# Kernel tuning notes

Measured on AMD Instinct MI355X. Metric: run time of the kernel, lower is better.

The kernel has to match this reference:

```python
import jax, jax.numpy as jnp
import numpy as np

NUM_NODES = 100000
D = 256            # node_hidden_dim
H = 256            # edge_hidden_dim
P = 524288         # num_pairs


def setup_inputs() -> dict:
    key = jax.random.key(0)
    k1, k2, k3, k4, k5, k6 = jax.random.split(key, 6)
    h_nodes = jax.random.normal(k1, (NUM_NODES, D), dtype=jnp.float32)
    dst = jax.random.randint(k2, (P,), 0, NUM_NODES, dtype=jnp.int64)
    src = jax.random.randint(k3, (P,), 0, NUM_NODES, dtype=jnp.int64)
    # Bias-free MLP weights, stored as [in, out] so forward is x @ W
    s1 = 1.0 / np.sqrt(2 * D)
    s2 = 1.0 / np.sqrt(H)
    W1 = jax.random.uniform(k4, (2 * D, H), jnp.float32, -s1, s1)
    W2 = jax.random.uniform(k5, (H, H), jnp.float32, -s2, s2)
    W3 = jax.random.uniform(k6, (H, 2), jnp.float32, -s2, s2)
    return {"h_nodes": h_nodes, "dst": dst, "src": src, "W1": W1, "W2": W2, "W3": W3}


def reference(h_nodes, dst, src, W1, W2, W3):
    # gather src/dst embeddings and concat -> [P, 2D]
    h_pair = jnp.concatenate([h_nodes[dst], h_nodes[src]], axis=-1)
    x = jax.nn.relu(h_pair @ W1)   # [P, H]
    x = jax.nn.relu(x @ W2)        # [P, H]
    return x @ W3                  # [P, 2] edge logits
```

## Files before the change

kernel.cpp:

```cpp
#include <hip/hip_runtime.h>
#include <stdint.h>

typedef __attribute__((ext_vector_type(8))) short short8;
typedef __attribute__((ext_vector_type(4))) float floatx4;

__device__ __forceinline__ unsigned short f2bf(float x) {
  unsigned int u = __float_as_uint(x);
  u += 0x7fffu + ((u >> 16) & 1u);
  return (unsigned short)(u >> 16);
}
__device__ __forceinline__ float bf2f(unsigned short b) {
  return __uint_as_float(((unsigned int)b) << 16);
}

__global__ void hcvt_kernel(const float* __restrict__ h,
                            unsigned short* __restrict__ o, int total8) {
  int u = blockIdx.x * 256 + threadIdx.x;
  if (u >= total8) return;
  const float4* h4 = (const float4*)h;
  float4 v0 = h4[u * 2], v1 = h4[u * 2 + 1];
  short8 s;
  s[0] = (short)f2bf(v0.x); s[1] = (short)f2bf(v0.y);
  s[2] = (short)f2bf(v0.z); s[3] = (short)f2bf(v0.w);
  s[4] = (short)f2bf(v1.x); s[5] = (short)f2bf(v1.y);
  s[6] = (short)f2bf(v1.z); s[7] = (short)f2bf(v1.w);
  ((short8*)o)[u] = s;
}

__global__ void wfrag_kernel(const float* __restrict__ W,
                             unsigned short* __restrict__ out, int total) {
  int u = blockIdx.x * 256 + threadIdx.x;
  if (u >= total) return;
  int j   = u & 7;
  int kq  = (u >> 3) & 3;
  int n   = (u >> 5) & 255;
  int k32 = u >> 13;
  int k   = k32 * 32 + kq * 8 + j;
  out[u] = f2bf(W[k * 256 + n]);
}

__global__ __launch_bounds__(256, 2)
void edge_mlp2(const unsigned short* __restrict__ hbf,
               const int* __restrict__ dst,
               const int* __restrict__ src,
               const unsigned short* __restrict__ W1F,
               const unsigned short* __restrict__ W2F,
               const float* __restrict__ W3,
               float* __restrict__ out) {
  __shared__ unsigned short A[64 * 512];
  __shared__ float w3s[512];
  __shared__ int ioff[128];
  unsigned short* X = A;

  const int t = threadIdx.x, lane = t & 63, w = t >> 6;
  const int lq = lane >> 4, lm = lane & 15;
  const int m0 = blockIdx.x * 64;

  if (t < 64)       ioff[t] = dst[m0 + t];
  else if (t < 128) ioff[t] = src[m0 + t - 64];
  w3s[t] = W3[t];
  w3s[t + 256] = W3[t + 256];
  __syncthreads();

  {
    const int c = lane, half = (c >= 32) ? 64 : 0, cc = c & 31;
    short8 g[16];
#pragma unroll
    for (int it = 0; it < 16; ++it) {
      int node = ioff[half + it * 4 + w];
      g[it] = ((const short8*)hbf)[node * 32 + cc];
    }
#pragma unroll
    for (int it = 0; it < 16; ++it) {
      int r = it * 4 + w;
      *(short8*)&A[r * 512 + ((c ^ (r & 7)) << 3)] = g[it];
    }
  }

  floatx4 acc[4][4];
#pragma unroll
  for (int i = 0; i < 4; ++i)
#pragma unroll
    for (int j = 0; j < 4; ++j) acc[i][j] = (floatx4)(0.0f);
  __syncthreads();

  const short8* B1 = (const short8*)W1F;
  const short8* B2 = (const short8*)W2F;

  {
    short8 bq[4][4];
#pragma unroll
    for (int s = 0; s < 4; ++s)
#pragma unroll
      for (int jt = 0; jt < 4; ++jt)
        bq[s][jt] = B1[(s * 256 + w * 64 + jt * 16 + lm) * 4 + lq];

#pragma unroll
    for (int s = 0; s < 16; ++s) {
#pragma unroll
      for (int i = 0; i < 4; ++i) {
        int r = i * 16 + lm, cch = s * 4 + lq;
        short8 af = *(const short8*)&A[r * 512 + ((cch ^ (r & 7)) << 3)];
#pragma unroll
        for (int j = 0; j < 4; ++j)
          acc[i][j] = __builtin_amdgcn_mfma_f32_16x16x32_bf16(af, bq[s & 3][j], acc[i][j], 0, 0, 0);
      }
      if (s < 12)
#pragma unroll
        for (int jt = 0; jt < 4; ++jt)
          bq[s & 3][jt] = B1[((s + 4) * 256 + w * 64 + jt * 16 + lm) * 4 + lq];
    }
  }
  __syncthreads();
#pragma unroll
  for (int i = 0; i < 4; ++i) {
    int row0 = i * 16 + lq * 4;
#pragma unroll
    for (int j = 0; j < 4; ++j) {
      int col = w * 64 + j * 16 + lm, c8 = col >> 3, ce = col & 7;
#pragma unroll
      for (int rg = 0; rg < 4; ++rg) {
        int row = row0 + rg;
        float v = acc[i][j][rg];
        v = v > 0.0f ? v : 0.0f;
        X[row * 256 + (((c8 ^ (row & 7)) << 3) | ce)] = f2bf(v);
      }
    }
  }
#pragma unroll
  for (int i = 0; i < 4; ++i)
#pragma unroll
    for (int j = 0; j < 4; ++j) acc[i][j] = (floatx4)(0.0f);
  __syncthreads();

  {
    short8 bq[4][4];
#pragma unroll
    for (int s = 0; s < 4; ++s)
#pragma unroll
      for (int jt = 0; jt < 4; ++jt)
        bq[s][jt] = B2[(s * 256 + w * 64 + jt * 16 + lm) * 4 + lq];

#pragma unroll
    for (int s = 0; s < 8; ++s) {
#pragma unroll
      for (int i = 0; i < 4; ++i) {
        int r = i * 16 + lm, cch = s * 4 + lq;
        short8 af = *(const short8*)&X[r * 256 + ((cch ^ (r & 7)) << 3)];
#pragma unroll
        for (int j = 0; j < 4; ++j)
          acc[i][j] = __builtin_amdgcn_mfma_f32_16x16x32_bf16(af, bq[s & 3][j], acc[i][j], 0, 0, 0);
      }
      if (s < 4)
#pragma unroll
        for (int jt = 0; jt < 4; ++jt)
          bq[s & 3][jt] = B2[((s + 4) * 256 + w * 64 + jt * 16 + lm) * 4 + lq];
    }
  }
  __syncthreads();
#pragma unroll
  for (int i = 0; i < 4; ++i) {
    int row0 = i * 16 + lq * 4;
#pragma unroll
    for (int j = 0; j < 4; ++j) {
      int col = w * 64 + j * 16 + lm, c8 = col >> 3, ce = col & 7;
#pragma unroll
      for (int rg = 0; rg < 4; ++rg) {
        int row = row0 + rg;
        float v = acc[i][j][rg];
        v = v > 0.0f ? v : 0.0f;
        X[row * 256 + (((c8 ^ (row & 7)) << 3) | ce)] = f2bf(v);
      }
    }
  }
  __syncthreads();

  {
    int r = t >> 2, o = (t >> 1) & 1, hh = t & 1;
    float s = 0.0f;
#pragma unroll
    for (int it = 0; it < 16; ++it) {
      int c = hh * 16 + it;
      short8 xv = *(const short8*)&X[r * 256 + ((c ^ (r & 7)) << 3)];
#pragma unroll
      for (int e = 0; e < 8; ++e)
        s += bf2f((unsigned short)xv[e]) * w3s[((c << 3) + e) * 2 + o];
    }
    s += __shfl_xor(s, 1);
    if (hh == 0) out[(m0 + r) * 2 + o] = s;
  }
}

__global__ __launch_bounds__(256, 2)
void edge_mlp_fb(const float* __restrict__ h,
                 const int* __restrict__ dst,
                 const int* __restrict__ src,
                 const unsigned short* __restrict__ W1F,
                 const unsigned short* __restrict__ W2F,
                 const float* __restrict__ W3,
                 float* __restrict__ out) {
  __shared__ unsigned short A[64 * 512];
  __shared__ float w3s[512];
  __shared__ int ioff[128];
  unsigned short* X = A;
  const int t = threadIdx.x, lane = t & 63, w = t >> 6;
  const int lq = lane >> 4, lm = lane & 15;
  const int m0 = blockIdx.x * 64;
  if (t < 64) ioff[t] = dst[m0 + t];
  else if (t < 128) ioff[t] = src[m0 + t - 64];
  w3s[t] = W3[t];
  w3s[t + 256] = W3[t + 256];
  __syncthreads();
  {
    const int c = lane, half = (c >= 32) ? 64 : 0, cc = c & 31;
#pragma unroll
    for (int it = 0; it < 16; ++it) {
      int r = it * 4 + w;
      int node = ioff[half + r];
      const float4* h4 = (const float4*)h;
      float4 v0 = h4[node * 64 + cc * 2], v1 = h4[node * 64 + cc * 2 + 1];
      short8 v;
      v[0] = (short)f2bf(v0.x); v[1] = (short)f2bf(v0.y);
      v[2] = (short)f2bf(v0.z); v[3] = (short)f2bf(v0.w);
      v[4] = (short)f2bf(v1.x); v[5] = (short)f2bf(v1.y);
      v[6] = (short)f2bf(v1.z); v[7] = (short)f2bf(v1.w);
      *(short8*)&A[r * 512 + ((c ^ (r & 7)) << 3)] = v;
    }
  }
  floatx4 acc[4][4];
#pragma unroll
  for (int i = 0; i < 4; ++i)
#pragma unroll
    for (int j = 0; j < 4; ++j) acc[i][j] = (floatx4)(0.0f);
  __syncthreads();
  const short8* B1 = (const short8*)W1F;
  const short8* B2 = (const short8*)W2F;
#pragma unroll
  for (int k32 = 0; k32 < 16; ++k32) {
    short8 b[4], af[4];
#pragma unroll
    for (int jt = 0; jt < 4; ++jt)
      b[jt] = B1[(k32 * 256 + w * 64 + jt * 16 + lm) * 4 + lq];
#pragma unroll
    for (int i = 0; i < 4; ++i) {
      int r = i * 16 + lm, c = k32 * 4 + lq;
      af[i] = *(const short8*)&A[r * 512 + ((c ^ (r & 7)) << 3)];
    }
#pragma unroll
    for (int i = 0; i < 4; ++i)
#pragma unroll
      for (int j = 0; j < 4; ++j)
        acc[i][j] = __builtin_amdgcn_mfma_f32_16x16x32_bf16(af[i], b[j], acc[i][j], 0, 0, 0);
  }
  __syncthreads();
#pragma unroll
  for (int i = 0; i < 4; ++i) {
    int row0 = i * 16 + lq * 4;
#pragma unroll
    for (int j = 0; j < 4; ++j) {
      int col = w * 64 + j * 16 + lm, c8 = col >> 3, ce = col & 7;
#pragma unroll
      for (int rg = 0; rg < 4; ++rg) {
        int row = row0 + rg;
        float v = acc[i][j][rg];
        v = v > 0.0f ? v : 0.0f;
        X[row * 256 + (((c8 ^ (row & 7)) << 3) | ce)] = f2bf(v);
      }
    }
  }
#pragma unroll
  for (int i = 0; i < 4; ++i)
#pragma unroll
    for (int j = 0; j < 4; ++j) acc[i][j] = (floatx4)(0.0f);
  __syncthreads();
#pragma unroll
  for (int k32 = 0; k32 < 8; ++k32) {
    short8 b[4], af[4];
#pragma unroll
    for (int jt = 0; jt < 4; ++jt)
      b[jt] = B2[(k32 * 256 + w * 64 + jt * 16 + lm) * 4 + lq];
#pragma unroll
    for (int i = 0; i < 4; ++i) {
      int r = i * 16 + lm, c = k32 * 4 + lq;
      af[i] = *(const short8*)&X[r * 256 + ((c ^ (r & 7)) << 3)];
    }
#pragma unroll
    for (int i = 0; i < 4; ++i)
#pragma unroll
      for (int j = 0; j < 4; ++j)
        acc[i][j] = __builtin_amdgcn_mfma_f32_16x16x32_bf16(af[i], b[j], acc[i][j], 0, 0, 0);
  }
  __syncthreads();
#pragma unroll
  for (int i = 0; i < 4; ++i) {
    int row0 = i * 16 + lq * 4;
#pragma unroll
    for (int j = 0; j < 4; ++j) {
      int col = w * 64 + j * 16 + lm, c8 = col >> 3, ce = col & 7;
#pragma unroll
      for (int rg = 0; rg < 4; ++rg) {
        int row = row0 + rg;
        float v = acc[i][j][rg];
        v = v > 0.0f ? v : 0.0f;
        X[row * 256 + (((c8 ^ (row & 7)) << 3) | ce)] = f2bf(v);
      }
    }
  }
  __syncthreads();
  {
    int r = t >> 2, o = (t >> 1) & 1, hh = t & 1;
    float s = 0.0f;
#pragma unroll
    for (int it = 0; it < 16; ++it) {
      int c = hh * 16 + it;
      short8 xv = *(const short8*)&X[r * 256 + ((c ^ (r & 7)) << 3)];
#pragma unroll
      for (int e = 0; e < 8; ++e)
        s += bf2f((unsigned short)xv[e]) * w3s[((c << 3) + e) * 2 + o];
    }
    s += __shfl_xor(s, 1);
    if (hh == 0) out[(m0 + r) * 2 + o] = s;
  }
}

extern "C" void kernel_launch(void* const* d_in, const int* in_sizes, int n_in,
                              void* d_out, int out_size, void* d_ws, size_t ws_size,
                              hipStream_t stream) {
  const float* h   = (const float*)d_in[0];
  const int*   dst = (const int*)d_in[1];
  const int*   src = (const int*)d_in[2];
  const float* W1  = (const float*)d_in[3];
  const float* W2  = (const float*)d_in[4];
  const float* W3  = (const float*)d_in[5];
  float* out = (float*)d_out;

  const int h_elems = in_sizes[0];
  const int n_pairs = in_sizes[1];
  const int ntiles  = n_pairs / 64;

  const size_t hbf_elems = (size_t)h_elems;
  const bool use_hbf = ws_size >= (hbf_elems + 131072 + 65536) * sizeof(unsigned short);

  unsigned short* HBF = (unsigned short*)d_ws;
  unsigned short* W1F = use_hbf ? HBF + hbf_elems : (unsigned short*)d_ws;
  unsigned short* W2F = W1F + 131072;

  wfrag_kernel<<<512, 256, 0, stream>>>(W1, W1F, 131072);
  wfrag_kernel<<<256, 256, 0, stream>>>(W2, W2F, 65536);

  if (use_hbf) {
    int total8 = h_elems / 8;
    hcvt_kernel<<<(total8 + 255) / 256, 256, 0, stream>>>(h, HBF, total8);
    edge_mlp2<<<ntiles, 256, 0, stream>>>(HBF, dst, src, W1F, W2F, W3, out);
  } else {
    edge_mlp_fb<<<ntiles, 256, 0, stream>>>(h, dst, src, W1F, W2F, W3, out);
  }
}
```

Baseline: 416.3 us.

## Merge prep kernels, use MFMA for final layer, change LDS swizzle

Combines the W1/W2 fragment conversion and the h-to-bf16 conversion into a single prep launch, and adds a padded bf16 W3 fragment so the final 256x2 projection runs as one MFMA chain per wave instead of a scalar dot product with shared-memory W3. The LDS XOR swizzle is changed to also depend on row bit 3, which aims to reduce bank conflicts. The second-layer output is written to a separate LDS region. Together these aim to cut launch overhead, the scalar tail, and LDS conflicts, at the cost of an extra workspace buffer and a final MFMA that mostly computes zero padding.

```diff
diff --git a/kernel.cpp b/kernel.cpp
--- a/kernel.cpp
+++ b/kernel.cpp
@@ -2,6 +2,7 @@
 #include <stdint.h>
 
 typedef __attribute__((ext_vector_type(8))) short short8;
+typedef __attribute__((ext_vector_type(4))) short short4v;
 typedef __attribute__((ext_vector_type(4))) float floatx4;
 
 __device__ __forceinline__ unsigned short f2bf(float x) {
@@ -12,183 +13,205 @@
 __device__ __forceinline__ float bf2f(unsigned short b) {
   return __uint_as_float(((unsigned int)b) << 16);
 }
-
-__global__ void hcvt_kernel(const float* __restrict__ h,
-                            unsigned short* __restrict__ o, int total8) {
-  int u = blockIdx.x * 256 + threadIdx.x;
-  if (u >= total8) return;
-  const float4* h4 = (const float4*)h;
-  float4 v0 = h4[u * 2], v1 = h4[u * 2 + 1];
-  short8 s;
-  s[0] = (short)f2bf(v0.x); s[1] = (short)f2bf(v0.y);
-  s[2] = (short)f2bf(v0.z); s[3] = (short)f2bf(v0.w);
-  s[4] = (short)f2bf(v1.x); s[5] = (short)f2bf(v1.y);
-  s[6] = (short)f2bf(v1.z); s[7] = (short)f2bf(v1.w);
-  ((short8*)o)[u] = s;
+__device__ __forceinline__ int sw3(int r) { return (r & 7) ^ (((r >> 3) & 1) * 3); }
+
+__global__ void prep_kernel(const float* __restrict__ h, const float* __restrict__ W1,
+                            const float* __restrict__ W2, const float* __restrict__ W3,
+                            unsigned short* __restrict__ HBF, unsigned short* __restrict__ W1F,
+                            unsigned short* __restrict__ W2F, unsigned short* __restrict__ W3F,
+                            int nh4) {
+  const int t = threadIdx.x;
+  int b = blockIdx.x;
+  if (b < 512) {
+    int u = b * 256 + t;
+    int j = u & 7, kq = (u >> 3) & 3, n = (u >> 5) & 255, k32 = u >> 13;
+    W1F[u] = f2bf(W1[(k32 * 32 + kq * 8 + j) * 256 + n]);
+    return;
+  }
+  b -= 512;
+  if (b < 256) {
+    int u = b * 256 + t;
+    int j = u & 7, kq = (u >> 3) & 3, n = (u >> 5) & 255, k32 = u >> 13;
+    W2F[u] = f2bf(W2[(k32 * 32 + kq * 8 + j) * 256 + n]);
+    return;
+  }
+  b -= 256;
+  if (b < 16) {
+    int u = b * 256 + t;
+    int j = u & 7, L = (u >> 3) & 63, k32 = u >> 9;
+    int n = L & 15, kq = L >> 4;
+    W3F[u] = (n < 2) ? f2bf(W3[(k32 * 32 + kq * 8 + j) * 2 + n]) : (unsigned short)0;
+    return;
+  }
+  b -= 16;
+  int u = b * 256 + t;
+  if (u < nh4) {
+    float4 v = ((const float4*)h)[u];
+    short4v s;
+    s[0] = (short)f2bf(v.x); s[1] = (short)f2bf(v.y);
+    s[2] = (short)f2bf(v.z); s[3] = (short)f2bf(v.w);
+    ((short4v*)HBF)[u] = s;
+  }
+}
+
+__global__ __launch_bounds__(256, 2)
+void edge_mlp3(const unsigned short* __restrict__ hbf,
+               const int* __restrict__ dst,
+               const int* __restrict__ src,
+               const unsigned short* __restrict__ W1F,
+               const unsigned short* __restrict__ W2F,
+               const unsigned short* __restrict__ W3F,
+               float* __restrict__ out) {
+  __shared__ unsigned short A[64 * 512];
+  __shared__ int ioff[128];
+  unsigned short* X  = A;
+  unsigned short* X2 = A + 16384;
+
+  const int t = threadIdx.x, lane = t & 63, w = t >> 6;
+  const int lq = lane >> 4, lm = lane & 15;
+  const int m0 = blockIdx.x * 64;
+
+  if (t < 64)       ioff[t] = dst[m0 + t];
+  else if (t < 128) ioff[t] = src[m0 + t - 64];
+  __syncthreads();
+
+  {
+    const int c = lane, half = (c >= 32) ? 64 : 0, cc = c & 31;
+    short8 g[16];
+#pragma unroll
+    for (int it = 0; it < 16; ++it) {
+      int node = ioff[half + it * 4 + w];
+      g[it] = ((const short8*)hbf)[node * 32 + cc];
+    }
+#pragma unroll
+    for (int it = 0; it < 16; ++it) {
+      int r = it * 4 + w;
+      *(short8*)&A[r * 512 + ((c ^ sw3(r)) << 3)] = g[it];
+    }
+  }
+
+  floatx4 acc[4][4];
+#pragma unroll
+  for (int i = 0; i < 4; ++i)
+#pragma unroll
+    for (int j = 0; j < 4; ++j) acc[i][j] = (floatx4)(0.0f);
+  __syncthreads();
+
+  const short8* B1 = (const short8*)W1F;
+  const short8* B2 = (const short8*)W2F;
+
+  {
+    short8 bq[4][4];
+#pragma unroll
+    for (int s = 0; s < 4; ++s)
+#pragma unroll
+      for (int jt = 0; jt < 4; ++jt)
+        bq[s][jt] = B1[(s * 256 + w * 64 + jt * 16 + lm) * 4 + lq];
+
+#pragma unroll
+    for (int s = 0; s < 16; ++s) {
+#pragma unroll
+      for (int i = 0; i < 4; ++i) {
+        int r = i * 16 + lm, cch = s * 4 + lq;
+        short8 af = *(const short8*)&A[r * 512 + ((cch ^ sw3(r)) << 3)];
+#pragma unroll
+        for (int j = 0; j < 4; ++j)
+          acc[i][j] = __builtin_amdgcn_mfma_f32_16x16x32_bf16(af, bq[s & 3][j], acc[i][j], 0, 0, 0);
+      }
+      if (s < 12)
+#pragma unroll
+        for (int jt = 0; jt < 4; ++jt)
+          bq[s & 3][jt] = B1[((s + 4) * 256 + w * 64 + jt * 16 + lm) * 4 + lq];
+    }
+  }
+  __syncthreads();
+#pragma unroll
+  for (int i = 0; i < 4; ++i) {
+    int row0 = i * 16 + lq * 4;
+#pragma unroll
+    for (int j = 0; j < 4; ++j) {
+      int col = w * 64 + j * 16 + lm, c8 = col >> 3, ce = col & 7;
+#pragma unroll
+      for (int rg = 0; rg < 4; ++rg) {
+        int row = row0 + rg;
+        float v = acc[i][j][rg];
+        v = v > 0.0f ? v : 0.0f;
+        X[row * 256 + (((c8 ^ sw3(row)) << 3) | ce)] = f2bf(v);
+      }
+    }
+  }
+#pragma unroll
+  for (int i = 0; i < 4; ++i)
+#pragma unroll
+    for (int j = 0; j < 4; ++j) acc[i][j] = (floatx4)(0.0f);
+  __syncthreads();
+
+  {
+    short8 bq[4][4];
+#pragma unroll
+    for (int s = 0; s < 4; ++s)
+#pragma unroll
+      for (int jt = 0; jt < 4; ++jt)
+        bq[s][jt] = B2[(s * 256 + w * 64 + jt * 16 + lm) * 4 + lq];
+
+#pragma unroll
+    for (int s = 0; s < 8; ++s) {
+#pragma unroll
+      for (int i = 0; i < 4; ++i) {
+        int r = i * 16 + lm, cch = s * 4 + lq;
+        short8 af = *(const short8*)&X[r * 256 + ((cch ^ sw3(r)) << 3)];
+#pragma unroll
+        for (int j = 0; j < 4; ++j)
+          acc[i][j] = __builtin_amdgcn_mfma_f32_16x16x32_bf16(af, bq[s & 3][j], acc[i][j], 0, 0, 0);
+      }
+      if (s < 4)
+#pragma unroll
+        for (int jt = 0; jt < 4; ++jt)
+          bq[s & 3][jt] = B2[((s + 4) * 256 + w * 64 + jt * 16 + lm) * 4 + lq];
+    }
+  }
+  __syncthreads();
+#pragma unroll
+  for (int i = 0; i < 4; ++i) {
+    int row0 = i * 16 + lq * 4;
+#pragma unroll
+    for (int j = 0; j < 4; ++j) {
+      int col = w * 64 + j * 16 + lm, c8 = col >> 3, ce = col & 7;
+#pragma unroll
+      for (int rg = 0; rg < 4; ++rg) {
+        int row = row0 + rg;
+        float v = acc[i][j][rg];
+        v = v > 0.0f ? v : 0.0f;
+        X2[row * 256 + (((c8 ^ sw3(row)) << 3) | ce)] = f2bf(v);
+      }
+    }
+  }
+  __syncthreads();
+
+  {
+    floatx4 a3 = (floatx4)(0.0f);
+    const short8* B3 = (const short8*)W3F;
+#pragma unroll
+    for (int s = 0; s < 8; ++s) {
+      short8 b3 = B3[s * 64 + lane];
+      int r = w * 16 + lm, cch = s * 4 + lq;
+      short8 af = *(const short8*)&X2[r * 256 + ((cch ^ sw3(r)) << 3)];
+      a3 = __builtin_amdgcn_mfma_f32_16x16x32_bf16(af, b3, a3, 0, 0, 0);
+    }
+    if (lm < 2) {
+#pragma unroll
+      for (int rg = 0; rg < 4; ++rg)
+        out[(m0 + w * 16 + lq * 4 + rg) * 2 + lm] = a3[rg];
+    }
+  }
 }
 
 __global__ void wfrag_kernel(const float* __restrict__ W,
                              unsigned short* __restrict__ out, int total) {
   int u = blockIdx.x * 256 + threadIdx.x;
   if (u >= total) return;
-  int j   = u & 7;
-  int kq  = (u >> 3) & 3;
-  int n   = (u >> 5) & 255;
-  int k32 = u >> 13;
-  int k   = k32 * 32 + kq * 8 + j;
-  out[u] = f2bf(W[k * 256 + n]);
-}
-
-__global__ __launch_bounds__(256, 2)
-void edge_mlp2(const unsigned short* __restrict__ hbf,
-               const int* __restrict__ dst,
-               const int* __restrict__ src,
-               const unsigned short* __restrict__ W1F,
-               const unsigned short* __restrict__ W2F,
-               const float* __restrict__ W3,
-               float* __restrict__ out) {
-  __shared__ unsigned short A[64 * 512];
-  __shared__ float w3s[512];
-  __shared__ int ioff[128];
-  unsigned short* X = A;
-
-  const int t = threadIdx.x, lane = t & 63, w = t >> 6;
-  const int lq = lane >> 4, lm = lane & 15;
-  const int m0 = blockIdx.x * 64;
-
-  if (t < 64)       ioff[t] = dst[m0 + t];
-  else if (t < 128) ioff[t] = src[m0 + t - 64];
-  w3s[t] = W3[t];
-  w3s[t + 256] = W3[t + 256];
-  __syncthreads();
-
-  {
-    const int c = lane, half = (c >= 32) ? 64 : 0, cc = c & 31;
-    short8 g[16];
-#pragma unroll
-    for (int it = 0; it < 16; ++it) {
-      int node = ioff[half + it * 4 + w];
-      g[it] = ((const short8*)hbf)[node * 32 + cc];
-    }
-#pragma unroll
-    for (int it = 0; it < 16; ++it) {
-      int r = it * 4 + w;
-      *(short8*)&A[r * 512 + ((c ^ (r & 7)) << 3)] = g[it];
-    }
-  }
-
-  floatx4 acc[4][4];
-#pragma unroll
-  for (int i = 0; i < 4; ++i)
-#pragma unroll
-    for (int j = 0; j < 4; ++j) acc[i][j] = (floatx4)(0.0f);
-  __syncthreads();
-
-  const short8* B1 = (const short8*)W1F;
-  const short8* B2 = (const short8*)W2F;
-
-  {
-    short8 bq[4][4];
-#pragma unroll
-    for (int s = 0; s < 4; ++s)
-#pragma unroll
-      for (int jt = 0; jt < 4; ++jt)
-        bq[s][jt] = B1[(s * 256 + w * 64 + jt * 16 + lm) * 4 + lq];
-
-#pragma unroll
-    for (int s = 0; s < 16; ++s) {
-#pragma unroll
-      for (int i = 0; i < 4; ++i) {
-        int r = i * 16 + lm, cch = s * 4 + lq;
-        short8 af = *(const short8*)&A[r * 512 + ((cch ^ (r & 7)) << 3)];
-#pragma unroll
-        for (int j = 0; j < 4; ++j)
-          acc[i][j] = __builtin_amdgcn_mfma_f32_16x16x32_bf16(af, bq[s & 3][j], acc[i][j], 0, 0, 0);
-      }
-      if (s < 12)
-#pragma unroll
-        for (int jt = 0; jt < 4; ++jt)
-          bq[s & 3][jt] = B1[((s + 4) * 256 + w * 64 + jt * 16 + lm) * 4 + lq];
-    }
-  }
-  __syncthreads();
-#pragma unroll
-  for (int i = 0; i < 4; ++i) {
-    int row0 = i * 16 + lq * 4;
-#pragma unroll
-    for (int j = 0; j < 4; ++j) {
-      int col = w * 64 + j * 16 + lm, c8 = col >> 3, ce = col & 7;
-#pragma unroll
-      for (int rg = 0; rg < 4; ++rg) {
-        int row = row0 + rg;
-        float v = acc[i][j][rg];
-        v = v > 0.0f ? v : 0.0f;
-        X[row * 256 + (((c8 ^ (row & 7)) << 3) | ce)] = f2bf(v);
-      }
-    }
-  }
-#pragma unroll
-  for (int i = 0; i < 4; ++i)
-#pragma unroll
-    for (int j = 0; j < 4; ++j) acc[i][j] = (floatx4)(0.0f);
-  __syncthreads();
-
-  {
-    short8 bq[4][4];
-#pragma unroll
-    for (int s = 0; s < 4; ++s)
-#pragma unroll
-      for (int jt = 0; jt < 4; ++jt)
-        bq[s][jt] = B2[(s * 256 + w * 64 + jt * 16 + lm) * 4 + lq];
-
-#pragma unroll
-    for (int s = 0; s < 8; ++s) {
-#pragma unroll
-      for (int i = 0; i < 4; ++i) {
-        int r = i * 16 + lm, cch = s * 4 + lq;
-        short8 af = *(const short8*)&X[r * 256 + ((cch ^ (r & 7)) << 3)];
-#pragma unroll
-        for (int j = 0; j < 4; ++j)
-          acc[i][j] = __builtin_amdgcn_mfma_f32_16x16x32_bf16(af, bq[s & 3][j], acc[i][j], 0, 0, 0);
-      }
-      if (s < 4)
-#pragma unroll
-        for (int jt = 0; jt < 4; ++jt)
-          bq[s & 3][jt] = B2[((s + 4) * 256 + w * 64 + jt * 16 + lm) * 4 + lq];
-    }
-  }
-  __syncthreads();
-#pragma unroll
-  for (int i = 0; i < 4; ++i) {
-    int row0 = i * 16 + lq * 4;
-#pragma unroll
-    for (int j = 0; j < 4; ++j) {
-      int col = w * 64 + j * 16 + lm, c8 = col >> 3, ce = col & 7;
-#pragma unroll
-      for (int rg = 0; rg < 4; ++rg) {
-        int row = row0 + rg;
-        float v = acc[i][j][rg];
-        v = v > 0.0f ? v : 0.0f;
-        X[row * 256 + (((c8 ^ (row & 7)) << 3) | ce)] = f2bf(v);
-      }
-    }
-  }
-  __syncthreads();
-
-  {
-    int r = t >> 2, o = (t >> 1) & 1, hh = t & 1;
-    float s = 0.0f;
-#pragma unroll
-    for (int it = 0; it < 16; ++it) {
-      int c = hh * 16 + it;
-      short8 xv = *(const short8*)&X[r * 256 + ((c ^ (r & 7)) << 3)];
-#pragma unroll
-      for (int e = 0; e < 8; ++e)
-        s += bf2f((unsigned short)xv[e]) * w3s[((c << 3) + e) * 2 + o];
-    }
-    s += __shfl_xor(s, 1);
-    if (hh == 0) out[(m0 + r) * 2 + o] = s;
-  }
+  int j = u & 7, kq = (u >> 3) & 3, n = (u >> 5) & 255, k32 = u >> 13;
+  out[u] = f2bf(W[(k32 * 32 + kq * 8 + j) * 256 + n]);
 }
 
 __global__ __launch_bounds__(256, 2)
@@ -339,20 +362,24 @@
   const int ntiles  = n_pairs / 64;
 
   const size_t hbf_elems = (size_t)h_elems;
-  const bool use_hbf = ws_size >= (hbf_elems + 131072 + 65536) * sizeof(unsigned short);
+  const bool use_hbf =
+      ws_size >= (hbf_elems + 131072 + 65536 + 4096) * sizeof(unsigned short);
 
   unsigned short* HBF = (unsigned short*)d_ws;
-  unsigned short* W1F = use_hbf ? HBF + hbf_elems : (unsigned short*)d_ws;
+  unsigned short* W1F = HBF + hbf_elems;
   unsigned short* W2F = W1F + 131072;
-
-  wfrag_kernel<<<512, 256, 0, stream>>>(W1, W1F, 131072);
-  wfrag_kernel<<<256, 256, 0, stream>>>(W2, W2F, 65536);
+  unsigned short* W3F = W2F + 65536;
 
   if (use_hbf) {
-    int total8 = h_elems / 8;
-    hcvt_kernel<<<(total8 + 255) / 256, 256, 0, stream>>>(h, HBF, total8);
-    edge_mlp2<<<ntiles, 256, 0, stream>>>(HBF, dst, src, W1F, W2F, W3, out);
+    int nh4 = h_elems / 4;
+    int grid = 512 + 256 + 16 + (nh4 + 255) / 256;
+    prep_kernel<<<grid, 256, 0, stream>>>(h, W1, W2, W3, HBF, W1F, W2F, W3F, nh4);
+    edge_mlp3<<<ntiles, 256, 0, stream>>>(HBF, dst, src, W1F, W2F, W3F, out);
   } else {
-    edge_mlp_fb<<<ntiles, 256, 0, stream>>>(h, dst, src, W1F, W2F, W3, out);
-  }
-}
+    unsigned short* W1Fb = (unsigned short*)d_ws;
+    unsigned short* W2Fb = W1Fb + 131072;
+    wfrag_kernel<<<512, 256, 0, stream>>>(W1, W1Fb, 131072);
+    wfrag_kernel<<<256, 256, 0, stream>>>(W2, W2Fb, 65536);
+    edge_mlp_fb<<<ntiles, 256, 0, stream>>>(h, dst, src, W1Fb, W2Fb, W3, out);
+  }
+}
```

Result: no change. 410.1 us (-1.5%).
